# Optimization experiments

Measured on AMD Instinct MI355X. Metric: run time of the kernel, lower is better.

Reference implementation:

```python
import jax, jax.numpy as jnp
import numpy as np
from jax import lax

TOP_K = 8
N_EXPERTS = 256
N_GROUP = 8
TOPK_GROUP = 4
ROUTED_SCALING = 2.5
NORM_TOPK_PROB = True


def setup_inputs() -> dict:
    key = jax.random.key(0)
    k1, k2, k3 = jax.random.split(key, 3)
    hidden_states = jax.random.normal(k1, (4, 4096, 4096), dtype=jnp.float32)
    weight = jax.random.normal(k2, (N_EXPERTS, 4096), dtype=jnp.float32) * 0.02
    e_score_correction_bias = jax.random.normal(k3, (N_EXPERTS,), dtype=jnp.float32) * 0.1
    return {
        "hidden_states": hidden_states,
        "weight": weight,
        "e_score_correction_bias": e_score_correction_bias,
    }


def reference(hidden_states, weight, e_score_correction_bias):
    bsz, seq_len, h = hidden_states.shape
    T = bsz * seq_len
    x = hidden_states.reshape(T, h).astype(jnp.float32)
    # gate GEMM: [T, h] x [E, h]^T -> [T, E]
    logits = jnp.einsum("th,eh->te", x, weight.astype(jnp.float32))
    scores = jax.nn.sigmoid(logits)

    scores_for_choice = scores + e_score_correction_bias[None, :]  # [T, E]
    eg = N_EXPERTS // N_GROUP  # experts per group
    grp = scores_for_choice.reshape(T, N_GROUP, eg)
    top2, _ = lax.top_k(grp, 2)                      # [T, G, 2]
    group_scores = top2.sum(axis=-1)                  # [T, G]
    _, group_idx = lax.top_k(group_scores, TOPK_GROUP)  # [T, topk_group]
    group_mask = jnp.zeros((T, N_GROUP), dtype=scores.dtype)
    group_mask = group_mask.at[jnp.arange(T)[:, None], group_idx].set(1.0)
    score_mask = jnp.broadcast_to(group_mask[:, :, None], (T, N_GROUP, eg)).reshape(T, N_EXPERTS)

    neg_inf = jnp.float32(-jnp.inf)
    tmp_scores = jnp.where(score_mask > 0, scores_for_choice, neg_inf)
    _, topk_idx = lax.top_k(tmp_scores, TOP_K)        # [T, top_k]
    topk_weight = jnp.take_along_axis(scores, topk_idx, axis=1)

    if TOP_K > 1 and NORM_TOPK_PROB:
        denom = topk_weight.sum(axis=-1, keepdims=True) + 1e-20
        topk_weight = topk_weight / denom
    topk_weight = topk_weight * ROUTED_SCALING
    return topk_idx, topk_weight
```

## Files before the change

kernel.cpp:

```cpp
#include <hip/hip_runtime.h>
#include <math.h>

#define Hdim 4096
#define NE 256
#define BM 32
#define BK 32
#define NKC (Hdim / BK)
#define PLANE_ELEMS (Hdim * NE)
#define CHUNK_ELEMS 8192

#define C0 9.765625e-4f
#define C1 4.76837158203125e-7f

typedef _Float16 f16x8 __attribute__((ext_vector_type(8)));
typedef _Float16 f16x4 __attribute__((ext_vector_type(4)));
typedef float f32x4 __attribute__((ext_vector_type(4)));

#define KBAR()                                               \
  {                                                          \
    asm volatile("s_waitcnt lgkmcnt(0)" ::: "memory");       \
    __builtin_amdgcn_s_barrier();                            \
  }

__global__ __launch_bounds__(256)
void convert_w(const float* __restrict__ W, _Float16* __restrict__ pl) {
  const int id = blockIdx.x * 256 + threadIdx.x;
  const int k8 = id & 511;
  const int n = id >> 9;
  const float* src = W + (long)n * Hdim + k8 * 8;
  const float4 x0 = *(const float4*)src;
  const float4 x1 = *(const float4*)(src + 4);
  const float xv[8] = {x0.x, x0.y, x0.z, x0.w, x1.x, x1.y, x1.z, x1.w};
  f16x8 vh, vm;
#pragma unroll
  for (int j = 0; j < 8; ++j) {
    const float v = xv[j] * 64.f;
    const _Float16 h = (_Float16)v;
    const float r = (v - (float)h) * 2048.f;
    vh[j] = h;
    vm[j] = (_Float16)r;
  }
  const long co = ((long)k8 * NE + n) * 8;
  *(f16x8*)(pl + co) = vh;
  *(f16x8*)(pl + PLANE_ELEMS + co) = vm;
}

__global__ __launch_bounds__(512, 4)
void moe_gate_fused(const float* __restrict__ X, const _Float16* __restrict__ pl,
                    const float* __restrict__ bias, float* __restrict__ out, int T) {
  __shared__ __align__(16) unsigned char smem[36864];
  const int tid = threadIdx.x;
  const int lane = tid & 63, wave = tid >> 6;
  const int r16 = lane & 15, c4 = lane >> 4;
  const long bm0 = (long)blockIdx.x * BM;

  f32x4 acc0[2][2], acc1[2][2];
#pragma unroll
  for (int i = 0; i < 2; ++i)
#pragma unroll
    for (int j = 0; j < 2; ++j) {
      acc0[i][j] = (f32x4)(0.f);
      acc1[i][j] = (f32x4)(0.f);
    }

  const int xm = tid >> 4;
  const int xf = tid & 15;
  const float* xsrc = X + (bm0 + xm) * (long)Hdim + xf * 4;
  const int xws = (xf >> 3) * 4096 +
                  (((xf & 7) >> 1) * 32 + xm) * 16 + (xf & 1) * 8;

  const _Float16* wsrc0 = pl + ((size_t)(c4 * 256 + wave * 32 + r16)) * 8;
  const _Float16* wsrc1 = wsrc0 + PLANE_ELEMS;

  f16x8 wA[2][2], wB[2][2], wC[2][2], wD[2][2];

#define LOADW(dst, kc_)                                                         \
  {                                                                             \
    const size_t ko = (size_t)(kc_) * CHUNK_ELEMS;                              \
    _Pragma("unroll") for (int fn = 0; fn < 2; ++fn) {                          \
      dst[0][fn] = *(const f16x8*)(wsrc0 + ko + fn * 128);                      \
      dst[1][fn] = *(const f16x8*)(wsrc1 + ko + fn * 128);                      \
    }                                                                           \
  }

#define WRITE_X2(b, xr)                                                         \
  {                                                                             \
    f16x4 vh, vm;                                                               \
    const float xa[4] = {(xr).x, (xr).y, (xr).z, (xr).w};                       \
    _Pragma("unroll") for (int j = 0; j < 4; ++j) {                             \
      const float v = xa[j] * 16.f;                                             \
      const _Float16 h = (_Float16)v;                                           \
      const float r = (v - (float)h) * 2048.f;                                  \
      vh[j] = h;                                                                \
      vm[j] = (_Float16)r;                                                      \
    }                                                                           \
    const int xo = (b) * 8192 + xws;                                            \
    *(f16x4*)&smem[xo] = vh;                                                    \
    *(f16x4*)&smem[xo + 2048] = vm;                                             \
  }

#define COMPUTE(b, sc, wreg)                                                    \
  {                                                                             \
    const int xo = (b) * 8192 + (sc) * 4096;                                    \
    f16x8 af[2][2];                                                             \
    _Pragma("unroll") for (int p = 0; p < 2; ++p)                               \
        _Pragma("unroll") for (int fm = 0; fm < 2; ++fm)                        \
            af[p][fm] = *(const f16x8*)&smem[xo + p * 2048 +                    \
                                             (c4 * 32 + fm * 16 + r16) * 16];   \
    _Pragma("unroll") for (int fm = 0; fm < 2; ++fm)                            \
        _Pragma("unroll") for (int fn = 0; fn < 2; ++fn) {                      \
      acc0[fm][fn] = __builtin_amdgcn_mfma_f32_16x16x32_f16(                    \
          af[0][fm], wreg[0][fn], acc0[fm][fn], 0, 0, 0);                       \
      f32x4 s = acc1[fm][fn];                                                   \
      s = __builtin_amdgcn_mfma_f32_16x16x32_f16(af[0][fm], wreg[1][fn], s, 0, 0, 0); \
      s = __builtin_amdgcn_mfma_f32_16x16x32_f16(af[1][fm], wreg[0][fn], s, 0, 0, 0); \
      acc1[fm][fn] = s;                                                         \
    }                                                                           \
  }

  {
    const float4 x0 = *(const float4*)(xsrc);
    WRITE_X2(0, x0);
  }
  LOADW(wA, 0);
  LOADW(wB, 1);
  __syncthreads();

  for (int p = 0; p < NKC / 2; p += 2) {
    {
      const float4 xn = *(const float4*)(xsrc + (size_t)(p + 1) * 64);
      LOADW(wC, 2 * p + 2);
      LOADW(wD, 2 * p + 3);
      __builtin_amdgcn_sched_barrier(0);
      COMPUTE(0, 0, wA);
      COMPUTE(0, 1, wB);
      WRITE_X2(1, xn);
      KBAR();
    }
    {
      const int pn = (p + 2 < NKC / 2) ? p + 2 : NKC / 2 - 1;
      const float4 xn = *(const float4*)(xsrc + (size_t)pn * 64);
      LOADW(wA, 2 * pn);
      LOADW(wB, 2 * pn + 1);
      __builtin_amdgcn_sched_barrier(0);
      COMPUTE(1, 0, wC);
      COMPUTE(1, 1, wD);
      if (p + 2 < NKC / 2) WRITE_X2(0, xn);
      KBAR();
    }
  }

  __syncthreads();
  float* lg = (float*)smem;
#pragma unroll
  for (int fm = 0; fm < 2; ++fm)
#pragma unroll
    for (int fn = 0; fn < 2; ++fn)
#pragma unroll
      for (int r = 0; r < 4; ++r) {
        const int t = fm * 16 + c4 * 4 + r;
        const int n = wave * 32 + fn * 16 + r16;
        lg[t * 260 + n] = fmaf(acc1[fm][fn][r], C1, acc0[fm][fn][r] * C0);
      }
  __syncthreads();

  const float4 bv = *(const float4*)(bias + lane * 4);
  for (int i = 0; i < 4; ++i) {
    const int t = wave * 4 + i;
    const float4 lgv = *(const float4*)&lg[t * 260 + lane * 4];

    const float s0 = 1.f / (1.f + expf(-lgv.x));
    const float s1 = 1.f / (1.f + expf(-lgv.y));
    const float s2 = 1.f / (1.f + expf(-lgv.z));
    const float s3 = 1.f / (1.f + expf(-lgv.w));

    const float c0 = s0 + bv.x, c1 = s1 + bv.y, c2 = s2 + bv.z, c3 = s3 + bv.w;

    float m1 = fmaxf(c0, c1), m2 = fminf(c0, c1);
    if (c2 > m1) { m2 = m1; m1 = c2; } else m2 = fmaxf(m2, c2);
    if (c3 > m1) { m2 = m1; m1 = c3; } else m2 = fmaxf(m2, c3);
#pragma unroll
    for (int off = 1; off < 8; off <<= 1) {
      const float o1 = __shfl_xor(m1, off);
      const float o2 = __shfl_xor(m2, off);
      if (o1 > m1) { m2 = fmaxf(m1, o2); m1 = o1; }
      else m2 = fmaxf(m2, o1);
    }
    const float gs = m1 + m2;

    const int gme = lane >> 3;
    int rank = 0;
#pragma unroll
    for (int j = 0; j < 8; ++j) {
      const float gj = __shfl(gs, j * 8);
      rank += ((gj > gs) || (gj == gs && j < gme)) ? 1 : 0;
    }
    const bool sel = rank < 4;

    const float NEG = -INFINITY;
    float q0 = sel ? c0 : NEG, q1 = sel ? c1 : NEG;
    float q2 = sel ? c2 : NEG, q3 = sel ? c3 : NEG;

    float sum = 0.f;
    int my_e = 0;
    float my_w = 0.f;
#pragma unroll
    for (int r = 0; r < 8; ++r) {
      float v = q0; int ix = 0;
      if (q1 > v) { v = q1; ix = 1; }
      if (q2 > v) { v = q2; ix = 2; }
      if (q3 > v) { v = q3; ix = 3; }
      int e = lane * 4 + ix;
#pragma unroll
      for (int off = 1; off < 64; off <<= 1) {
        const float v2 = __shfl_xor(v, off);
        const int e2 = __shfl_xor(e, off);
        const bool take = (v2 > v) || (v2 == v && e2 < e);
        v = take ? v2 : v;
        e = take ? e2 : e;
      }
      const int slot = e & 3, owner = e >> 2;
      const float svs = (slot == 0) ? s0 : ((slot == 1) ? s1 : ((slot == 2) ? s2 : s3));
      const float wgt = __shfl(svs, owner);
      sum += wgt;
      if (lane == r) { my_e = e; my_w = wgt; }
      const bool own = (lane == owner);
      q0 = (own && slot == 0) ? NEG : q0;
      q1 = (own && slot == 1) ? NEG : q1;
      q2 = (own && slot == 2) ? NEG : q2;
      q3 = (own && slot == 3) ? NEG : q3;
    }

    if (lane < 8) {
      const float denom = sum + 1e-20f;
      const long tg = bm0 + t;
      out[tg * 8 + lane] = (float)my_e;
      out[(long)T * 8 + tg * 8 + lane] = my_w / denom * 2.5f;
    }
  }
}

extern "C" void kernel_launch(void* const* d_in, const int* in_sizes, int n_in,
                              void* d_out, int out_size, void* d_ws, size_t ws_size,
                              hipStream_t stream) {
  const float* X = (const float*)d_in[0];
  const float* W = (const float*)d_in[1];
  const float* B = (const float*)d_in[2];
  float* out = (float*)d_out;
  const int T = in_sizes[0] / Hdim;

  _Float16* planes = (_Float16*)d_ws;

  convert_w<<<512, 256, 0, stream>>>(W, planes);
  moe_gate_fused<<<T / BM, 512, 0, stream>>>(X, planes, B, out, T);
}
```

Baseline: 162.6 us.

## Double token tile to 64 rows per block to halve weight-plane reloads

Raises the token tile from 32 to 64 rows. Each wave now holds 4x2 accumulator fragments, and every weight register load is reused across twice as many tokens. The X staging layout, the LDS buffers and the weight double-buffering are reorganised, and each block now needs 66.5KB of LDS. The aim is to cut the L2/global traffic from reloading the split-f16 weight planes. The trade-offs are half as many blocks, a lower occupancy hint, and higher register and LDS pressure, which could hurt latency hiding.

```diff
diff --git a/kernel.cpp b/kernel.cpp
--- a/kernel.cpp
+++ b/kernel.cpp
@@ -3,7 +3,7 @@
 
 #define Hdim 4096
 #define NE 256
-#define BM 32
+#define BM 64
 #define BK 32
 #define NKC (Hdim / BK)
 #define PLANE_ELEMS (Hdim * NE)
@@ -45,107 +45,115 @@
   *(f16x8*)(pl + PLANE_ELEMS + co) = vm;
 }
 
-__global__ __launch_bounds__(512, 4)
+__global__ __launch_bounds__(512, 2)
 void moe_gate_fused(const float* __restrict__ X, const _Float16* __restrict__ pl,
                     const float* __restrict__ bias, float* __restrict__ out, int T) {
-  __shared__ __align__(16) unsigned char smem[36864];
+  __shared__ __align__(16) unsigned char smem[66560];
   const int tid = threadIdx.x;
   const int lane = tid & 63, wave = tid >> 6;
   const int r16 = lane & 15, c4 = lane >> 4;
   const long bm0 = (long)blockIdx.x * BM;
 
-  f32x4 acc0[2][2], acc1[2][2];
-#pragma unroll
-  for (int i = 0; i < 2; ++i)
+  f32x4 acc0[4][2], acc1[4][2];
+#pragma unroll
+  for (int i = 0; i < 4; ++i)
 #pragma unroll
     for (int j = 0; j < 2; ++j) {
       acc0[i][j] = (f32x4)(0.f);
       acc1[i][j] = (f32x4)(0.f);
     }
 
-  const int xm = tid >> 4;
-  const int xf = tid & 15;
-  const float* xsrc = X + (bm0 + xm) * (long)Hdim + xf * 4;
-  const int xws = (xf >> 3) * 4096 +
-                  (((xf & 7) >> 1) * 32 + xm) * 16 + (xf & 1) * 8;
+  const int xm = tid >> 3;
+  const int f4 = tid & 7;
+  const float* xsrc = X + (bm0 + xm) * (long)Hdim + f4 * 4;
+  const int k8w = f4 >> 1, hw = f4 & 1;
+  const int xws = k8w * 1024 + xm * 16 + hw * 8;
 
   const _Float16* wsrc0 = pl + ((size_t)(c4 * 256 + wave * 32 + r16)) * 8;
   const _Float16* wsrc1 = wsrc0 + PLANE_ELEMS;
 
-  f16x8 wA[2][2], wB[2][2], wC[2][2], wD[2][2];
-
-#define LOADW(dst, kc_)                                                         \
-  {                                                                             \
-    const size_t ko = (size_t)(kc_) * CHUNK_ELEMS;                              \
-    _Pragma("unroll") for (int fn = 0; fn < 2; ++fn) {                          \
-      dst[0][fn] = *(const f16x8*)(wsrc0 + ko + fn * 128);                      \
-      dst[1][fn] = *(const f16x8*)(wsrc1 + ko + fn * 128);                      \
+  f16x8 wA[2][2][2], wB[2][2][2];
+
+#define LOADW(dst, pair_)                                                       \
+  {                                                                             \
+    _Pragma("unroll") for (int sc = 0; sc < 2; ++sc) {                          \
+      const size_t ko = (size_t)((pair_) * 2 + sc) * CHUNK_ELEMS;               \
+      _Pragma("unroll") for (int fn = 0; fn < 2; ++fn) {                        \
+        dst[sc][0][fn] = *(const f16x8*)(wsrc0 + ko + fn * 128);                \
+        dst[sc][1][fn] = *(const f16x8*)(wsrc1 + ko + fn * 128);                \
+      }                                                                         \
     }                                                                           \
   }
 
-#define WRITE_X2(b, xr)                                                         \
-  {                                                                             \
-    f16x4 vh, vm;                                                               \
-    const float xa[4] = {(xr).x, (xr).y, (xr).z, (xr).w};                       \
-    _Pragma("unroll") for (int j = 0; j < 4; ++j) {                             \
-      const float v = xa[j] * 16.f;                                             \
-      const _Float16 h = (_Float16)v;                                           \
-      const float r = (v - (float)h) * 2048.f;                                  \
-      vh[j] = h;                                                                \
-      vm[j] = (_Float16)r;                                                      \
+#define LOADX(pair_)                                                            \
+  {                                                                             \
+    xn0 = *(const float4*)(xsrc + (size_t)(pair_) * 64);                        \
+    xn1 = *(const float4*)(xsrc + (size_t)(pair_) * 64 + 32);                   \
+  }
+
+#define WRITE_X2(b, xr0, xr1)                                                   \
+  {                                                                             \
+    _Pragma("unroll") for (int sc = 0; sc < 2; ++sc) {                          \
+      const float4 xr = sc ? (xr1) : (xr0);                                     \
+      f16x4 vh, vm;                                                             \
+      const float xa[4] = {xr.x, xr.y, xr.z, xr.w};                             \
+      _Pragma("unroll") for (int j = 0; j < 4; ++j) {                           \
+        const float v = xa[j] * 16.f;                                           \
+        const _Float16 h = (_Float16)v;                                         \
+        const float r = (v - (float)h) * 2048.f;                                \
+        vh[j] = h;                                                              \
+        vm[j] = (_Float16)r;                                                    \
+      }                                                                         \
+      const int xo = (b) * 16384 + sc * 8192 + xws;                             \
+      *(f16x4*)&smem[xo] = vh;                                                  \
+      *(f16x4*)&smem[xo + 4096] = vm;                                           \
     }                                                                           \
-    const int xo = (b) * 8192 + xws;                                            \
-    *(f16x4*)&smem[xo] = vh;                                                    \
-    *(f16x4*)&smem[xo + 2048] = vm;                                             \
   }
 
 #define COMPUTE(b, sc, wreg)                                                    \
   {                                                                             \
-    const int xo = (b) * 8192 + (sc) * 4096;                                    \
-    f16x8 af[2][2];                                                             \
+    const int xo = (b) * 16384 + (sc) * 8192;                                   \
+    f16x8 af[2][4];                                                             \
     _Pragma("unroll") for (int p = 0; p < 2; ++p)                               \
-        _Pragma("unroll") for (int fm = 0; fm < 2; ++fm)                        \
-            af[p][fm] = *(const f16x8*)&smem[xo + p * 2048 +                    \
-                                             (c4 * 32 + fm * 16 + r16) * 16];   \
-    _Pragma("unroll") for (int fm = 0; fm < 2; ++fm)                            \
+        _Pragma("unroll") for (int fm = 0; fm < 4; ++fm)                        \
+            af[p][fm] = *(const f16x8*)&smem[xo + p * 4096 + c4 * 1024 +        \
+                                             (fm * 16 + r16) * 16];             \
+    _Pragma("unroll") for (int fm = 0; fm < 4; ++fm)                            \
         _Pragma("unroll") for (int fn = 0; fn < 2; ++fn) {                      \
       acc0[fm][fn] = __builtin_amdgcn_mfma_f32_16x16x32_f16(                    \
-          af[0][fm], wreg[0][fn], acc0[fm][fn], 0, 0, 0);                       \
+          af[0][fm], wreg[sc][0][fn], acc0[fm][fn], 0, 0, 0);                   \
       f32x4 s = acc1[fm][fn];                                                   \
-      s = __builtin_amdgcn_mfma_f32_16x16x32_f16(af[0][fm], wreg[1][fn], s, 0, 0, 0); \
-      s = __builtin_amdgcn_mfma_f32_16x16x32_f16(af[1][fm], wreg[0][fn], s, 0, 0, 0); \
+      s = __builtin_amdgcn_mfma_f32_16x16x32_f16(af[0][fm], wreg[sc][1][fn], s, 0, 0, 0); \
+      s = __builtin_amdgcn_mfma_f32_16x16x32_f16(af[1][fm], wreg[sc][0][fn], s, 0, 0, 0); \
       acc1[fm][fn] = s;                                                         \
     }                                                                           \
   }
 
-  {
-    const float4 x0 = *(const float4*)(xsrc);
-    WRITE_X2(0, x0);
-  }
+  float4 xn0, xn1;
+
+  LOADX(0);
+  WRITE_X2(0, xn0, xn1);
   LOADW(wA, 0);
-  LOADW(wB, 1);
   __syncthreads();
 
   for (int p = 0; p < NKC / 2; p += 2) {
     {
-      const float4 xn = *(const float4*)(xsrc + (size_t)(p + 1) * 64);
-      LOADW(wC, 2 * p + 2);
-      LOADW(wD, 2 * p + 3);
+      LOADX(p + 1);
+      LOADW(wB, p + 1);
       __builtin_amdgcn_sched_barrier(0);
       COMPUTE(0, 0, wA);
-      COMPUTE(0, 1, wB);
-      WRITE_X2(1, xn);
+      COMPUTE(0, 1, wA);
+      WRITE_X2(1, xn0, xn1);
       KBAR();
     }
     {
       const int pn = (p + 2 < NKC / 2) ? p + 2 : NKC / 2 - 1;
-      const float4 xn = *(const float4*)(xsrc + (size_t)pn * 64);
-      LOADW(wA, 2 * pn);
-      LOADW(wB, 2 * pn + 1);
+      LOADX(pn);
+      LOADW(wA, pn);
       __builtin_amdgcn_sched_barrier(0);
-      COMPUTE(1, 0, wC);
-      COMPUTE(1, 1, wD);
-      if (p + 2 < NKC / 2) WRITE_X2(0, xn);
+      COMPUTE(1, 0, wB);
+      COMPUTE(1, 1, wB);
+      if (p + 2 < NKC / 2) WRITE_X2(0, xn0, xn1);
       KBAR();
     }
   }
@@ -153,7 +161,7 @@
   __syncthreads();
   float* lg = (float*)smem;
 #pragma unroll
-  for (int fm = 0; fm < 2; ++fm)
+  for (int fm = 0; fm < 4; ++fm)
 #pragma unroll
     for (int fn = 0; fn < 2; ++fn)
 #pragma unroll
@@ -165,8 +173,8 @@
   __syncthreads();
 
   const float4 bv = *(const float4*)(bias + lane * 4);
-  for (int i = 0; i < 4; ++i) {
-    const int t = wave * 4 + i;
+  for (int i = 0; i < 8; ++i) {
+    const int t = wave * 8 + i;
     const float4 lgv = *(const float4*)&lg[t * 260 + lane * 4];
 
     const float s0 = 1.f / (1.f + expf(-lgv.x));
```

Result: faster. 155.3 us (-4.5%).

## Double token tile to 64 rows with 1024-thread blocks and split W prefetch

Applied to the files above, without the earlier changes.

Raises the block tile from 32 to 64 tokens using 16 waves arranged 2x8, so each weight chunk fetched from global memory is reused across twice as many tokens. This halves total weight traffic from the fp16 planes. To stay within register limits at 1024 threads, the weight prefetch drops from four register buffers to two, interleaved between the two compute halves. Shared memory grows to about 65 KB, which limits occupancy to one block per CU and shortens the prefetch distance.

```diff
diff --git a/kernel.cpp b/kernel.cpp
--- a/kernel.cpp
+++ b/kernel.cpp
@@ -3,7 +3,7 @@
 
 #define Hdim 4096
 #define NE 256
-#define BM 32
+#define BM 64
 #define BK 32
 #define NKC (Hdim / BK)
 #define PLANE_ELEMS (Hdim * NE)
@@ -45,12 +45,13 @@
   *(f16x8*)(pl + PLANE_ELEMS + co) = vm;
 }
 
-__global__ __launch_bounds__(512, 4)
+__global__ __launch_bounds__(1024, 4)
 void moe_gate_fused(const float* __restrict__ X, const _Float16* __restrict__ pl,
                     const float* __restrict__ bias, float* __restrict__ out, int T) {
-  __shared__ __align__(16) unsigned char smem[36864];
+  __shared__ __align__(16) unsigned char smem[66560];
   const int tid = threadIdx.x;
-  const int lane = tid & 63, wave = tid >> 6;
+  const int lane = tid & 63, w = tid >> 6;
+  const int wm = w >> 3, wn = w & 7;
   const int r16 = lane & 15, c4 = lane >> 4;
   const long bm0 = (long)blockIdx.x * BM;
 
@@ -66,13 +67,14 @@
   const int xm = tid >> 4;
   const int xf = tid & 15;
   const float* xsrc = X + (bm0 + xm) * (long)Hdim + xf * 4;
-  const int xws = (xf >> 3) * 4096 +
-                  (((xf & 7) >> 1) * 32 + xm) * 16 + (xf & 1) * 8;
-
-  const _Float16* wsrc0 = pl + ((size_t)(c4 * 256 + wave * 32 + r16)) * 8;
+  const int sc_ = xf >> 3;
+  const int k8w = (xf & 7) >> 1, hw = xf & 1;
+  const int xws = sc_ * 8192 + k8w * 1024 + xm * 16 + hw * 8;
+
+  const _Float16* wsrc0 = pl + ((size_t)(c4 * 256 + wn * 32 + r16)) * 8;
   const _Float16* wsrc1 = wsrc0 + PLANE_ELEMS;
 
-  f16x8 wA[2][2], wB[2][2], wC[2][2], wD[2][2];
+  f16x8 wA[2][2], wB[2][2];
 
 #define LOADW(dst, kc_)                                                         \
   {                                                                             \
@@ -83,7 +85,9 @@
     }                                                                           \
   }
 
-#define WRITE_X2(b, xr)                                                         \
+#define LOADX(pair_) { xn0 = *(const float4*)(xsrc + (size_t)(pair_) * 64); }
+
+#define WRITE_X(b, xr)                                                          \
   {                                                                             \
     f16x4 vh, vm;                                                               \
     const float xa[4] = {(xr).x, (xr).y, (xr).z, (xr).w};                       \
@@ -94,19 +98,19 @@
       vh[j] = h;                                                                \
       vm[j] = (_Float16)r;                                                      \
     }                                                                           \
-    const int xo = (b) * 8192 + xws;                                            \
+    const int xo = (b) * 16384 + xws;                                           \
     *(f16x4*)&smem[xo] = vh;                                                    \
-    *(f16x4*)&smem[xo + 2048] = vm;                                             \
+    *(f16x4*)&smem[xo + 4096] = vm;                                             \
   }
 
 #define COMPUTE(b, sc, wreg)                                                    \
   {                                                                             \
-    const int xo = (b) * 8192 + (sc) * 4096;                                    \
+    const int xo = (b) * 16384 + (sc) * 8192;                                   \
     f16x8 af[2][2];                                                             \
     _Pragma("unroll") for (int p = 0; p < 2; ++p)                               \
         _Pragma("unroll") for (int fm = 0; fm < 2; ++fm)                        \
-            af[p][fm] = *(const f16x8*)&smem[xo + p * 2048 +                    \
-                                             (c4 * 32 + fm * 16 + r16) * 16];   \
+            af[p][fm] = *(const f16x8*)&smem[xo + p * 4096 + c4 * 1024 +        \
+                                             (wm * 32 + fm * 16 + r16) * 16];   \
     _Pragma("unroll") for (int fm = 0; fm < 2; ++fm)                            \
         _Pragma("unroll") for (int fn = 0; fn < 2; ++fn) {                      \
       acc0[fm][fn] = __builtin_amdgcn_mfma_f32_16x16x32_f16(                    \
@@ -118,34 +122,36 @@
     }                                                                           \
   }
 
-  {
-    const float4 x0 = *(const float4*)(xsrc);
-    WRITE_X2(0, x0);
-  }
+  float4 xn0;
+
+  LOADX(0);
+  WRITE_X(0, xn0);
   LOADW(wA, 0);
-  LOADW(wB, 1);
   __syncthreads();
 
   for (int p = 0; p < NKC / 2; p += 2) {
     {
-      const float4 xn = *(const float4*)(xsrc + (size_t)(p + 1) * 64);
-      LOADW(wC, 2 * p + 2);
-      LOADW(wD, 2 * p + 3);
+      LOADX(p + 1);
+      LOADW(wB, 2 * p + 1);
       __builtin_amdgcn_sched_barrier(0);
       COMPUTE(0, 0, wA);
+      LOADW(wA, 2 * p + 2);
+      __builtin_amdgcn_sched_barrier(0);
       COMPUTE(0, 1, wB);
-      WRITE_X2(1, xn);
+      WRITE_X(1, xn0);
       KBAR();
     }
     {
       const int pn = (p + 2 < NKC / 2) ? p + 2 : NKC / 2 - 1;
-      const float4 xn = *(const float4*)(xsrc + (size_t)pn * 64);
-      LOADW(wA, 2 * pn);
-      LOADW(wB, 2 * pn + 1);
-      __builtin_amdgcn_sched_barrier(0);
-      COMPUTE(1, 0, wC);
-      COMPUTE(1, 1, wD);
-      if (p + 2 < NKC / 2) WRITE_X2(0, xn);
+      LOADX(pn);
+      LOADW(wB, 2 * p + 3);
+      __builtin_amdgcn_sched_barrier(0);
+      COMPUTE(1, 0, wA);
+      const int kcn = (2 * p + 4 < NKC) ? 2 * p + 4 : NKC - 1;
+      LOADW(wA, kcn);
+      __builtin_amdgcn_sched_barrier(0);
+      COMPUTE(1, 1, wB);
+      if (p + 2 < NKC / 2) WRITE_X(0, xn0);
       KBAR();
     }
   }
@@ -158,15 +164,15 @@
     for (int fn = 0; fn < 2; ++fn)
 #pragma unroll
       for (int r = 0; r < 4; ++r) {
-        const int t = fm * 16 + c4 * 4 + r;
-        const int n = wave * 32 + fn * 16 + r16;
+        const int t = wm * 32 + fm * 16 + c4 * 4 + r;
+        const int n = wn * 32 + fn * 16 + r16;
         lg[t * 260 + n] = fmaf(acc1[fm][fn][r], C1, acc0[fm][fn][r] * C0);
       }
   __syncthreads();
 
   const float4 bv = *(const float4*)(bias + lane * 4);
   for (int i = 0; i < 4; ++i) {
-    const int t = wave * 4 + i;
+    const int t = w * 4 + i;
     const float4 lgv = *(const float4*)&lg[t * 260 + lane * 4];
 
     const float s0 = 1.f / (1.f + expf(-lgv.x));
@@ -252,5 +258,5 @@
   _Float16* planes = (_Float16*)d_ws;
 
   convert_w<<<512, 256, 0, stream>>>(W, planes);
-  moe_gate_fused<<<T / BM, 512, 0, stream>>>(X, planes, B, out, T);
+  moe_gate_fused<<<T / BM, 1024, 0, stream>>>(X, planes, B, out, T);
 }
```

Result: slower. 175.0 us (+7.6%).
